# Performance work log

Measured on AMD Instinct MI355X. Metric: run time of the kernel, lower is better.

The kernel has to match this reference:

```python
import jax, jax.numpy as jnp
import numpy as np

B, S, MV = 32, 64, 30
V, E, H, L = 20000, 256, 512, 128
PAD_IDX = 0
THETA = 0.5


def setup_inputs() -> dict:
    key = jax.random.key(0)
    ks = jax.random.split(key, 12)
    sc = 0.02
    return {
        "z": jax.random.normal(ks[0], (B, L), jnp.float32),
        "input_sequence": jax.random.randint(ks[1], (B, S, MV), 0, V),
        "length": jax.random.randint(ks[2], (B,), 1, S + 1),
        "embedding_weight": jax.random.normal(ks[3], (V, E), jnp.float32) * sc,
        "W_l2h": jax.random.normal(ks[4], (H, L), jnp.float32) * sc,
        "b_l2h": jax.random.normal(ks[5], (H,), jnp.float32) * sc,
        "W_ih": jax.random.normal(ks[6], (3 * H, E), jnp.float32) * sc,
        "W_hh": jax.random.normal(ks[7], (3 * H, H), jnp.float32) * sc,
        "b_ih": jax.random.normal(ks[8], (3 * H,), jnp.float32) * sc,
        "b_hh": jax.random.normal(ks[9], (3 * H,), jnp.float32) * sc,
        "W_out": jax.random.normal(ks[10], (V, H), jnp.float32) * sc,
        "b_out": jax.random.normal(ks[11], (V,), jnp.float32) * sc,
    }


def _gru(emb, h0, W_ih, W_hh, b_ih, b_hh):
    # emb: (B,S,E); PyTorch GRU cell, single layer.
    def step(h, x_t):
        gi = x_t @ W_ih.T + b_ih          # (B,3H)
        gh = h @ W_hh.T + b_hh            # (B,3H)
        i_r, i_z, i_n = jnp.split(gi, 3, axis=-1)
        h_r, h_z, h_n = jnp.split(gh, 3, axis=-1)
        r = jax.nn.sigmoid(i_r + h_r)
        zt = jax.nn.sigmoid(i_z + h_z)
        n = jnp.tanh(i_n + r * h_n)
        h_new = (1.0 - zt) * n + zt * h
        return h_new, h_new
    _, outs = jax.lax.scan(step, h0, jnp.swapaxes(emb, 0, 1))  # (S,B,H)
    return jnp.swapaxes(outs, 0, 1)  # (B,S,H)


def reference(z, input_sequence, length, embedding_weight, W_l2h, b_l2h,
              W_ih, W_hh, b_ih, b_hh, W_out, b_out):
    # Multi-hot scatter: zeros.scatter_(2, idx, 1)
    mh = jnp.zeros((B, S, V), jnp.float32).at[
        jnp.arange(B)[:, None, None], jnp.arange(S)[None, :, None], input_sequence
    ].set(1.0)
    mh = mh.at[:, :, PAD_IDX].set(0.0)
    # Dense one-hot matmul embedding-sum (faithful to torch.mm on (B*S,V))
    emb = jnp.tanh(jnp.einsum('bsv,ve->bse', mh, embedding_weight))
    h0 = z @ W_l2h.T + b_l2h                      # (B,H)
    outputs = _gru(emb, h0, W_ih, W_hh, b_ih, b_hh)  # (B,S,H)
    # pack/pad semantics: outputs beyond each length are zero
    valid = jnp.arange(S)[None, :] < length[:, None]
    outputs = outputs * valid[..., None]
    m_output = jnp.sum(jnp.abs(outputs), axis=2) > 0  # (B,S) bool
    logits = jnp.einsum('bsh,vh->bsv', outputs, W_out) + b_out  # (B,S,V)
    p_output = jax.nn.sigmoid(logits)
    # _sample: top-k over logits[..., 3:], shift by 3, threshold via sigmoid
    top_p, top_i = jax.lax.top_k(logits[..., 3:], MV)
    top_i = top_i + 3
    s_output = jnp.where(jax.nn.sigmoid(top_p) <= THETA, PAD_IDX, top_i)  # (B,S,MV)
    return (p_output, s_output, m_output)
```

## Files before the change

### kernel.cpp

```cpp
#include <hip/hip_runtime.h>
#include <hip/hip_bf16.h>
#include <math.h>

#define B_ 32
#define S_ 64
#define MV_ 30
#define V_ 20000
#define E_ 256
#define H_ 512
#define L_ 128
#define H3_ 1536
#define BS_ 2048
#define NB4 256
#define NEG7 -3.0e38f
#define SENT 0xFFF8000000000000ULL

typedef __attribute__((ext_vector_type(8))) short short8v;
typedef __attribute__((ext_vector_type(4))) float f32x4;
typedef unsigned long long ull_;

__global__ __launch_bounds__(256) void k12(const int* __restrict__ seq,
                                           const float* __restrict__ Ew,
                                           const float* __restrict__ z,
                                           const float* __restrict__ Wl,
                                           const float* __restrict__ bl,
                                           double* __restrict__ emb,
                                           double* __restrict__ hstep) {
    __shared__ int sidx[MV_];
    int bid = blockIdx.x;
    int t = threadIdx.x;
    if (bid < BS_) {
        int row = bid;
        if (t < MV_) sidx[t] = seq[row * MV_ + t];
        __syncthreads();
        double acc = 0.0;
        for (int i = 0; i < MV_; ++i) {
            int id = sidx[i];
            if (id == 0) continue;
            bool dup = false;
            for (int q = 0; q < i; ++q) dup = dup || (sidx[q] == id);
            if (!dup) acc += (double)Ew[(size_t)id * E_ + t];
        }
        emb[(size_t)row * E_ + t] = tanh(acc);
    } else if (bid < BS_ + 64) {
        int o = (bid - BS_) * 256 + t;
        int b = o >> 9;
        int j = o & 511;
        const float4* zr = (const float4*)(z + (size_t)b * L_);
        const float4* wr = (const float4*)(Wl + (size_t)j * L_);
        double acc = (double)bl[j];
#pragma unroll
        for (int k = 0; k < L_ / 4; ++k) {
            float4 a = zr[k];
            float4 w = wr[k];
            acc += (double)a.x * (double)w.x + (double)a.y * (double)w.y
                 + (double)a.z * (double)w.z + (double)a.w * (double)w.w;
        }
        hstep[(size_t)(b >> 2) * 2048 + j * 4 + (b & 3)] = acc;
    } else {
        ull_* hs = (ull_*)hstep;
        size_t i = (size_t)(bid - (BS_ + 64)) * 1024 + (size_t)t * 4;
        hs[16384 + i + 0] = SENT;
        hs[16384 + i + 1] = SENT;
        hs[16384 + i + 2] = SENT;
        hs[16384 + i + 3] = SENT;
    }
}

__global__ __launch_bounds__(256) void k3_gi(const double* __restrict__ A,
                                             const float* __restrict__ Bm,
                                             const float* __restrict__ bih,
                                             double* __restrict__ gi) {
    __shared__ double As[16][66];
    __shared__ double Bs[16][66];
    int t = threadIdx.x;
    int n0 = blockIdx.x * 64;
    int m0 = blockIdx.y * 64;
    int tx = t & 15, ty = t >> 4;
    int ml = t >> 2;
    int kl = (t & 3) * 4;
    double acc[4][4];
#pragma unroll
    for (int i = 0; i < 4; ++i)
#pragma unroll
        for (int j = 0; j < 4; ++j) acc[i][j] = 0.0;

    for (int kt = 0; kt < 256; kt += 16) {
        double4 av = *(const double4*)(A + (size_t)(m0 + ml) * 256 + kt + kl);
        float4 bv = *(const float4*)(Bm + (size_t)(n0 + ml) * 256 + kt + kl);
        As[kl + 0][ml] = av.x; As[kl + 1][ml] = av.y; As[kl + 2][ml] = av.z; As[kl + 3][ml] = av.w;
        Bs[kl + 0][ml] = (double)bv.x; Bs[kl + 1][ml] = (double)bv.y;
        Bs[kl + 2][ml] = (double)bv.z; Bs[kl + 3][ml] = (double)bv.w;
        __syncthreads();
#pragma unroll
        for (int kk = 0; kk < 16; ++kk) {
            double2 a01 = *(const double2*)&As[kk][ty * 4];
            double2 a23 = *(const double2*)&As[kk][ty * 4 + 2];
            double2 b01 = *(const double2*)&Bs[kk][tx * 4];
            double2 b23 = *(const double2*)&Bs[kk][tx * 4 + 2];
            double am[4] = {a01.x, a01.y, a23.x, a23.y};
            double bn[4] = {b01.x, b01.y, b23.x, b23.y};
#pragma unroll
            for (int i = 0; i < 4; ++i)
#pragma unroll
                for (int j = 0; j < 4; ++j) acc[i][j] += am[i] * bn[j];
        }
        __syncthreads();
    }
#pragma unroll
    for (int i = 0; i < 4; ++i) {
        int m = m0 + ty * 4 + i;
        int bb = m >> 6, ss = m & 63;
#pragma unroll
        for (int j = 0; j < 4; ++j) {
            int n = n0 + tx * 4 + j;
            int g = n >> 9, u = n & 511;
            gi[(((size_t)(ss * 512 + u)) * 3 + g) * 32 + bb] = acc[i][j] + (double)bih[n];
        }
    }
}

__global__ __launch_bounds__(256, 1) void k4_gru(const double* __restrict__ gi,
                                                 const float* __restrict__ whh,
                                                 const float* __restrict__ bhh,
                                                 const int* __restrict__ length,
                                                 double* __restrict__ hstep,
                                                 float* __restrict__ outs,
                                                 short* __restrict__ A16) {
    __shared__ double hl[2112];
    __shared__ double part[2][4][16][13];

    int t = threadIdx.x;
    int wv = t >> 6;
    int lane = t & 63;
    int bid = blockIdx.x;
    int g = bid & 7;
    int beta = bid >> 3;

    int ul = lane >> 2, ks = lane & 3;

    const float* wbase = whh + ((size_t)(beta * 16 + ul)) * 512 + wv * 128 + ks * 32;
    float4 w0r[8], w1r[8], w2r[8];
#pragma unroll
    for (int c = 0; c < 8; ++c) {
        w0r[c] = *(const float4*)(wbase + c * 4);
        w1r[c] = *(const float4*)(wbase + 512 * 512 + c * 4);
        w2r[c] = *(const float4*)(wbase + 1024 * 512 + c * 4);
    }

    const double* hg0 = hstep + (size_t)g * 2048;
    {
#pragma unroll
        for (int j = 0; j < 8; ++j) {
            int e = t + j * 256;
            hl[e + ((e >> 7) << 2)] = hg0[e];
        }
    }
    __syncthreads();

    int u2 = lane >> 2, b2 = lane & 3;
    int u_g = beta * 16 + u2;
    int b_g = g * 4 + b2;
    double gr = 0.0, gz = 0.0, gn = 0.0, bhr_ = 0.0, bhz_ = 0.0, bhn_ = 0.0;
    double hv = 0.0;
    int len = 0;
    if (wv == 0) {
        bhr_ = (double)bhh[u_g];
        bhz_ = (double)bhh[u_g + 512];
        bhn_ = (double)bhh[u_g + 1024];
        len = length[b_g];
        hv = hg0[u_g * 4 + b2];
        size_t gb = ((size_t)u_g * 3) * 32 + b_g;
        gr = gi[gb]; gz = gi[gb + 32]; gn = gi[gb + 64];
    }

    const double* hr = &hl[(wv * 128 + ks * 32) * 4 + ((wv * 4 + ks) << 2)];

    for (int s = 0; s < S_; ++s) {
        int par = s & 1;
        ull_ ta[4], tb[4];
        const ull_* src = (const ull_*)(hstep + (size_t)s * 16384 + (size_t)g * 2048)
                          + wv * 512;
        if (s > 0) {
            while (true) {
                bool ok = true;
#pragma unroll
                for (int j = 0; j < 4; ++j) {
                    ta[j] = __hip_atomic_load(&src[(2 * j) * 64 + lane],
                                              __ATOMIC_RELAXED, __HIP_MEMORY_SCOPE_AGENT);
                    ok = ok && (ta[j] != SENT);
                }
                if (__all(ok)) break;
                __builtin_amdgcn_s_sleep(1);
            }
#pragma unroll
            for (int j = 0; j < 4; ++j)
                tb[j] = __hip_atomic_load(&src[(2 * j + 1) * 64 + lane],
                                          __ATOMIC_RELAXED, __HIP_MEMORY_SCOPE_AGENT);
            asm volatile("" ::: "memory");
            {
                ull_* hlu = (ull_*)hl;
#pragma unroll
                for (int j = 0; j < 4; ++j) {
                    int e = wv * 512 + (2 * j) * 64 + lane;
                    hlu[e + ((e >> 7) << 2)] = ta[j];
                }
            }
        }

        double a0[4] = {0, 0, 0, 0}, a1[4] = {0, 0, 0, 0}, a2[4] = {0, 0, 0, 0};
#pragma unroll
        for (int c = 0; c < 4; ++c) {
            const double* hp = hr + c * 16;
            double2 hA0 = *(const double2*)(hp + 0),  hB0 = *(const double2*)(hp + 2);
            double2 hA1 = *(const double2*)(hp + 4),  hB1 = *(const double2*)(hp + 6);
            double2 hA2 = *(const double2*)(hp + 8),  hB2 = *(const double2*)(hp + 10);
            double2 hA3 = *(const double2*)(hp + 12), hB3 = *(const double2*)(hp + 14);
            float4 w0 = w0r[c], w1 = w1r[c], w2 = w2r[c];
            { double d0 = (double)w0.x, d1 = (double)w1.x, d2 = (double)w2.x;
              a0[0] += hA0.x * d0; a0[1] += hA0.y * d0; a0[2] += hB0.x * d0; a0[3] += hB0.y * d0;
              a1[0] += hA0.x * d1; a1[1] += hA0.y * d1; a1[2] += hB0.x * d1; a1[3] += hB0.y * d1;
              a2[0] += hA0.x * d2; a2[1] += hA0.y * d2; a2[2] += hB0.x * d2; a2[3] += hB0.y * d2; }
            { double d0 = (double)w0.y, d1 = (double)w1.y, d2 = (double)w2.y;
              a0[0] += hA1.x * d0; a0[1] += hA1.y * d0; a0[2] += hB1.x * d0; a0[3] += hB1.y * d0;
              a1[0] += hA1.x * d1; a1[1] += hA1.y * d1; a1[2] += hB1.x * d1; a1[3] += hB1.y * d1;
              a2[0] += hA1.x * d2; a2[1] += hA1.y * d2; a2[2] += hB1.x * d2; a2[3] += hB1.y * d2; }
            { double d0 = (double)w0.z, d1 = (double)w1.z, d2 = (double)w2.z;
              a0[0] += hA2.x * d0; a0[1] += hA2.y * d0; a0[2] += hB2.x * d0; a0[3] += hB2.y * d0;
              a1[0] += hA2.x * d1; a1[1] += hA2.y * d1; a1[2] += hB2.x * d1; a1[3] += hB2.y * d1;
              a2[0] += hA2.x * d2; a2[1] += hA2.y * d2; a2[2] += hB2.x * d2; a2[3] += hB2.y * d2; }
            { double d0 = (double)w0.w, d1 = (double)w1.w, d2 = (double)w2.w;
              a0[0] += hA3.x * d0; a0[1] += hA3.y * d0; a0[2] += hB3.x * d0; a0[3] += hB3.y * d0;
              a1[0] += hA3.x * d1; a1[1] += hA3.y * d1; a1[2] += hB3.x * d1; a1[3] += hB3.y * d1;
              a2[0] += hA3.x * d2; a2[1] += hA3.y * d2; a2[2] += hB3.x * d2; a2[3] += hB3.y * d2; }
        }

        if (s > 0) {
            while (true) {
                bool ok = true;
#pragma unroll
                for (int j = 0; j < 4; ++j) ok = ok && (tb[j] != SENT);
                if (__all(ok)) break;
                __builtin_amdgcn_s_sleep(1);
#pragma unroll
                for (int j = 0; j < 4; ++j)
                    tb[j] = __hip_atomic_load(&src[(2 * j + 1) * 64 + lane],
                                              __ATOMIC_RELAXED, __HIP_MEMORY_SCOPE_AGENT);
            }
            asm volatile("" ::: "memory");
            {
                ull_* hlu = (ull_*)hl;
#pragma unroll
                for (int j = 0; j < 4; ++j) {
                    int e = wv * 512 + (2 * j + 1) * 64 + lane;
                    hlu[e + ((e >> 7) << 2)] = tb[j];
                }
            }
        }

#pragma unroll
        for (int c = 4; c < 8; ++c) {
            const double* hp = hr + c * 16;
            double2 hA0 = *(const double2*)(hp + 0),  hB0 = *(const double2*)(hp + 2);
            double2 hA1 = *(const double2*)(hp + 4),  hB1 = *(const double2*)(hp + 6);
            double2 hA2 = *(const double2*)(hp + 8),  hB2 = *(const double2*)(hp + 10);
            double2 hA3 = *(const double2*)(hp + 12), hB3 = *(const double2*)(hp + 14);
            float4 w0 = w0r[c], w1 = w1r[c], w2 = w2r[c];
            { double d0 = (double)w0.x, d1 = (double)w1.x, d2 = (double)w2.x;
              a0[0] += hA0.x * d0; a0[1] += hA0.y * d0; a0[2] += hB0.x * d0; a0[3] += hB0.y * d0;
              a1[0] += hA0.x * d1; a1[1] += hA0.y * d1; a1[2] += hB0.x * d1; a1[3] += hB0.y * d1;
              a2[0] += hA0.x * d2; a2[1] += hA0.y * d2; a2[2] += hB0.x * d2; a2[3] += hB0.y * d2; }
            { double d0 = (double)w0.y, d1 = (double)w1.y, d2 = (double)w2.y;
              a0[0] += hA1.x * d0; a0[1] += hA1.y * d0; a0[2] += hB1.x * d0; a0[3] += hB1.y * d0;
              a1[0] += hA1.x * d1; a1[1] += hA1.y * d1; a1[2] += hB1.x * d1; a1[3] += hB1.y * d1;
              a2[0] += hA1.x * d2; a2[1] += hA1.y * d2; a2[2] += hB1.x * d2; a2[3] += hB1.y * d2; }
            { double d0 = (double)w0.z, d1 = (double)w1.z, d2 = (double)w2.z;
              a0[0] += hA2.x * d0; a0[1] += hA2.y * d0; a0[2] += hB2.x * d0; a0[3] += hB2.y * d0;
              a1[0] += hA2.x * d1; a1[1] += hA2.y * d1; a1[2] += hB2.x * d1; a1[3] += hB2.y * d1;
              a2[0] += hA2.x * d2; a2[1] += hA2.y * d2; a2[2] += hB2.x * d2; a2[3] += hB2.y * d2; }
            { double d0 = (double)w0.w, d1 = (double)w1.w, d2 = (double)w2.w;
              a0[0] += hA3.x * d0; a0[1] += hA3.y * d0; a0[2] += hB3.x * d0; a0[3] += hB3.y * d0;
              a1[0] += hA3.x * d1; a1[1] += hA3.y * d1; a1[2] += hB3.x * d1; a1[3] += hB3.y * d1;
              a2[0] += hA3.x * d2; a2[1] += hA3.y * d2; a2[2] += hB3.x * d2; a2[3] += hB3.y * d2; }
        }

#pragma unroll
        for (int b = 0; b < 4; ++b) {
            a0[b] += __shfl_xor(a0[b], 1); a0[b] += __shfl_xor(a0[b], 2);
            a1[b] += __shfl_xor(a1[b], 1); a1[b] += __shfl_xor(a1[b], 2);
            a2[b] += __shfl_xor(a2[b], 1); a2[b] += __shfl_xor(a2[b], 2);
        }
        if (ks == 0) {
#pragma unroll
            for (int b = 0; b < 4; ++b) {
                part[par][wv][ul][0 * 4 + b] = a0[b];
                part[par][wv][ul][1 * 4 + b] = a1[b];
                part[par][wv][ul][2 * 4 + b] = a2[b];
            }
        }
        __syncthreads();

        if (wv == 0) {
            double s0 = part[par][0][u2][0 * 4 + b2] + part[par][1][u2][0 * 4 + b2]
                      + part[par][2][u2][0 * 4 + b2] + part[par][3][u2][0 * 4 + b2];
            double s1 = part[par][0][u2][1 * 4 + b2] + part[par][1][u2][1 * 4 + b2]
                      + part[par][2][u2][1 * 4 + b2] + part[par][3][u2][1 * 4 + b2];
            double s2 = part[par][0][u2][2 * 4 + b2] + part[par][1][u2][2 * 4 + b2]
                      + part[par][2][u2][2 * 4 + b2] + part[par][3][u2][2 * 4 + b2];
            double r  = 1.0 / (1.0 + exp(-(gr + s0 + bhr_)));
            double zt = 1.0 / (1.0 + exp(-(gz + s1 + bhz_)));
            double n  = tanh(gn + r * (s2 + bhn_));
            double hn_ = (1.0 - zt) * n + zt * hv;
            hv = hn_;
            if (s < S_ - 1) {
                ull_* hdst = (ull_*)(hstep + (size_t)(s + 1) * 16384 + (size_t)g * 2048);
                __hip_atomic_store(&hdst[beta * 64 + lane],
                                   __builtin_bit_cast(ull_, hn_),
                                   __ATOMIC_RELAXED, __HIP_MEMORY_SCOPE_AGENT);
                size_t gb = ((size_t)((s + 1) * 512 + u_g) * 3) * 32 + b_g;
                gr = gi[gb]; gz = gi[gb + 32]; gn = gi[gb + 64];
            }
            float ov = (s < len) ? (float)hn_ : 0.0f;
            size_t oidx = (size_t)(b_g * 64 + s) * H_ + u_g;
            outs[oidx] = ov;
            {
                unsigned u = __builtin_bit_cast(unsigned, ov);
                A16[oidx] = (short)((u + 0x7FFFu + ((u >> 16) & 1u)) >> 16);
            }
        }
    }
}

__device__ __forceinline__ unsigned short f2b_(float x) {
    unsigned u = __builtin_bit_cast(unsigned, x);
    return (unsigned short)((u + 0x7FFFu + ((u >> 16) & 1u)) >> 16);
}
__device__ __forceinline__ short8v pack8_(float4 a, float4 b) {
    short8v r;
    r[0] = (short)f2b_(a.x); r[1] = (short)f2b_(a.y);
    r[2] = (short)f2b_(a.z); r[3] = (short)f2b_(a.w);
    r[4] = (short)f2b_(b.x); r[5] = (short)f2b_(b.y);
    r[6] = (short)f2b_(b.z); r[7] = (short)f2b_(b.w);
    return r;
}
__global__ __launch_bounds__(256) void k_prep2(const float* __restrict__ Wsrc,
                                               short* __restrict__ W16) {
    int i = blockIdx.x * 256 + threadIdx.x;
    float4 a = *(const float4*)&Wsrc[(size_t)i * 8];
    float4 b = *(const float4*)&Wsrc[(size_t)i * 8 + 4];
    *(short8v*)&W16[(size_t)i * 8] = pack8_(a, b);
}

#define LDK5 72
__global__ __launch_bounds__(256, 2) void k5_mfma(const short* __restrict__ A16,
                                                  const short* __restrict__ W16,
                                                  const float* __restrict__ bo,
                                                  float* __restrict__ pOut) {
    __shared__ short As[128 * LDK5];
    __shared__ short Bs[128 * LDK5];
    int t = threadIdx.x;
    int bid = blockIdx.x;
    int swz = (bid & 7) * 314 + (bid >> 3);
    int m0 = (swz & 15) * 128;
    int n0 = (swz >> 4) * 128;
    int lane = t & 63, wv = t >> 6;
    int wr = wv >> 1, wc = wv & 1;
    int ml = t >> 1;
    int kl = (t & 1) * 32;

    const short* Arow = A16 + (size_t)(m0 + ml) * H_ + kl;
    int vrow = n0 + ml;
    bool vok = vrow < V_;
    const short* Wrow = W16 + (size_t)(vok ? vrow : 0) * H_ + kl;
    short8v zz = (short8v){0, 0, 0, 0, 0, 0, 0, 0};

    f32x4 acc[4][4];
#pragma unroll
    for (int i = 0; i < 4; ++i)
#pragma unroll
        for (int j = 0; j < 4; ++j) acc[i][j] = (f32x4){0.f, 0.f, 0.f, 0.f};

    int ko = lane >> 4;
    int rr = lane & 15;

    for (int kt = 0; kt < H_; kt += 64) {
        short8v a0 = *(const short8v*)(Arow + kt);
        short8v a1 = *(const short8v*)(Arow + kt + 8);
        short8v a2 = *(const short8v*)(Arow + kt + 16);
        short8v a3 = *(const short8v*)(Arow + kt + 24);
        short8v b0 = vok ? *(const short8v*)(Wrow + kt) : zz;
        short8v b1 = vok ? *(const short8v*)(Wrow + kt + 8) : zz;
        short8v b2 = vok ? *(const short8v*)(Wrow + kt + 16) : zz;
        short8v b3 = vok ? *(const short8v*)(Wrow + kt + 24) : zz;
        *(short8v*)&As[ml * LDK5 + kl]      = a0;
        *(short8v*)&As[ml * LDK5 + kl + 8]  = a1;
        *(short8v*)&As[ml * LDK5 + kl + 16] = a2;
        *(short8v*)&As[ml * LDK5 + kl + 24] = a3;
        *(short8v*)&Bs[ml * LDK5 + kl]      = b0;
        *(short8v*)&Bs[ml * LDK5 + kl + 8]  = b1;
        *(short8v*)&Bs[ml * LDK5 + kl + 16] = b2;
        *(short8v*)&Bs[ml * LDK5 + kl + 24] = b3;
        __syncthreads();

#pragma unroll
        for (int kh = 0; kh < 2; ++kh) {
            short8v af[4], bf[4];
#pragma unroll
            for (int i = 0; i < 4; ++i)
                af[i] = *(const short8v*)&As[(wr * 64 + i * 16 + rr) * LDK5 + kh * 32 + ko * 8];
#pragma unroll
            for (int j = 0; j < 4; ++j)
                bf[j] = *(const short8v*)&Bs[(wc * 64 + j * 16 + rr) * LDK5 + kh * 32 + ko * 8];
#pragma unroll
            for (int i = 0; i < 4; ++i)
#pragma unroll
                for (int j = 0; j < 4; ++j)
                    acc[i][j] = __builtin_amdgcn_mfma_f32_16x16x32_bf16(af[i], bf[j], acc[i][j], 0, 0, 0);
        }
        __syncthreads();
    }

    int cr4 = (lane >> 4) * 4;
    float bov[4];
#pragma unroll
    for (int j = 0; j < 4; ++j) {
        int v = n0 + wc * 64 + j * 16 + rr;
        bov[j] = (v < V_) ? bo[v] : 0.f;
    }
#pragma unroll
    for (int i = 0; i < 4; ++i) {
#pragma unroll
        for (int j = 0; j < 4; ++j) {
            int v = n0 + wc * 64 + j * 16 + rr;
            if (v < V_) {
#pragma unroll
                for (int r = 0; r < 4; ++r) {
                    int m = m0 + wr * 64 + i * 16 + cr4 + r;
                    float x = acc[i][j][r] + bov[j];
                    pOut[(size_t)m * V_ + v] = 1.0f / (1.0f + expf(-x));
                }
            }
        }
    }
}

__global__ __launch_bounds__(512) void k7a_cand(const float* __restrict__ pOut,
                                                float* __restrict__ candV,
                                                int* __restrict__ candI) {
    int row = blockIdx.x;
    int t = threadIdx.x;
    int wv = t >> 6;
    int lane = t & 63;
    const float* rowp = pOut + (size_t)row * V_ + wv * 2500;

    float rv[40];
#pragma unroll
    for (int q4 = 0; q4 < 10; ++q4) {
        int base = q4 * 256 + lane * 4;
        float4 v4 = *(const float4*)(rowp + base);
        float vv[4] = {v4.x, v4.y, v4.z, v4.w};
#pragma unroll
        for (int c = 0; c < 4; ++c) {
            int li = base + c;
            int col = wv * 2500 + li;
            bool ok = (li < 2500) && (col >= 3);
            rv[q4 * 4 + c] = ok ? vv[c] : NEG7;
        }
    }
    float m1 = rv[0]; int s1 = 0;
#pragma unroll
    for (int q = 1; q < 40; ++q)
        if (rv[q] > m1) { m1 = rv[q]; s1 = q; }
    float m2 = NEG7; int s2 = 0;
#pragma unroll
    for (int q = 0; q < 40; ++q)
        if (q != s1 && rv[q] > m2) { m2 = rv[q]; s2 = q; }
    bool dirty = false;
    ull_ used = 0;
    int myidx = wv * 2500 + (s1 >> 2) * 256 + lane * 4 + (s1 & 3);

    float keepv = NEG7; int keepi = 0;
#pragma unroll 1
    for (int r = 0; r < 32; ++r) {
        float bv = m1; int bi = myidx;
#pragma unroll
        for (int m = 1; m < 64; m <<= 1) {
            float ov = __shfl_xor(bv, m);
            int   oi = __shfl_xor(bi, m);
            if (ov > bv || (ov == bv && oi < bi)) { bv = ov; bi = oi; }
        }
        if (lane == r) { keepv = bv; keepi = bi; }
        if (myidx == bi) {
            used |= (1ull << s1);
            if (!dirty) {
                m1 = m2; s1 = s2; dirty = true;
            } else {
                m1 = NEG7; s1 = 0;
#pragma unroll
                for (int q = 0; q < 40; ++q) {
                    float v = ((used >> q) & 1ull) ? NEG7 : rv[q];
                    if (v > m1) { m1 = v; s1 = q; }
                }
                m2 = NEG7; s2 = 0;
#pragma unroll
                for (int q = 0; q < 40; ++q) {
                    float v = (((used >> q) & 1ull) || q == s1) ? NEG7 : rv[q];
                    if (v > m2) { m2 = v; s2 = q; }
                }
                dirty = false;
            }
            myidx = wv * 2500 + (s1 >> 2) * 256 + lane * 4 + (s1 & 3);
        }
    }
    if (lane < 32) {
        size_t o = ((size_t)row * 8 + wv) * 32 + lane;
        candV[o] = keepv;
        candI[o] = keepi;
    }
}

__global__ __launch_bounds__(256) void k7b_final(const float* __restrict__ candV,
                                                 const int* __restrict__ candI,
                                                 const float* __restrict__ outs,
                                                 const float* __restrict__ W,
                                                 const float* __restrict__ bo,
                                                 float* __restrict__ mOut,
                                                 float* __restrict__ sOut) {
    __shared__ float selv[64];
    __shared__ int   seli[64];
    __shared__ float resv[64];
    __shared__ float redm[4];
    __shared__ __align__(16) float orow[H_];

    int row = blockIdx.x;
    int t = threadIdx.x;
    int lane = t & 63, wid = t >> 6;

    if (wid != 0) {
        for (int i = t - 64; i < H_; i += 192)
            orow[i] = outs[(size_t)row * H_ + i];
    } else {
        float cv[4]; int ci[4];
#pragma unroll
        for (int q = 0; q < 4; ++q) {
            size_t o = (size_t)row * 256 + q * 64 + lane;
            cv[q] = candV[o];
            ci[q] = candI[o];
        }
        float lv = cv[0]; int lix = ci[0]; int ls = 0;
#pragma unroll
        for (int q = 1; q < 4; ++q)
            if (cv[q] > lv || (cv[q] == lv && ci[q] < lix)) { lv = cv[q]; lix = ci[q]; ls = q; }

#pragma unroll 1
        for (int r = 0; r < 64; ++r) {
            float bv = lv; int bi = lix;
#pragma unroll
            for (int m = 1; m < 64; m <<= 1) {
                float ov = __shfl_xor(bv, m);
                int   oi = __shfl_xor(bi, m);
                if (ov > bv || (ov == bv && oi < bi)) { bv = ov; bi = oi; }
            }
            if (lane == r) { selv[r] = bv; seli[r] = bi; }
            if (lix == bi) {
#pragma unroll
                for (int q = 0; q < 4; ++q) cv[q] = (ls == q) ? NEG7 : cv[q];
                lv = cv[0]; lix = ci[0]; ls = 0;
#pragma unroll
                for (int q = 1; q < 4; ++q)
                    if (cv[q] > lv || (cv[q] == lv && ci[q] < lix)) { lv = cv[q]; lix = ci[q]; ls = q; }
            }
        }
    }
    __syncthreads();

    {
        float ms = fabsf(orow[t]) + fabsf(orow[t + 256]);
#pragma unroll
        for (int m = 1; m < 64; m <<= 1) ms += __shfl_xor(ms, m);
        if (lane == 0) redm[wid] = ms;
    }

    {
        int c = t >> 2, q = t & 3;
        int gidx = seli[c];
        const float4* w4 = (const float4*)(W + (size_t)gidx * H_);
        const float4* o4 = (const float4*)orow;
        double acc = 0.0;
#pragma unroll 8
        for (int i2 = 0; i2 < 32; ++i2) {
            float4 wv4 = w4[i2 * 4 + q];
            float4 ov4 = o4[i2 * 4 + q];
            acc += (double)wv4.x * (double)ov4.x + (double)wv4.y * (double)ov4.y
                 + (double)wv4.z * (double)ov4.z + (double)wv4.w * (double)ov4.w;
        }
        acc += __shfl_xor(acc, 1);
        acc += __shfl_xor(acc, 2);
        if (q == 0) resv[c] = (float)(acc + (double)bo[gidx]);
    }
    __syncthreads();

    if (t == 0)
        mOut[row] = (redm[0] + redm[1] + redm[2] + redm[3] > 0.f) ? 1.f : 0.f;

    if (t < 64) {
        float v = resv[t];
        int idx = seli[t];
#pragma unroll 1
        for (int r = 0; r < MV_; ++r) {
            float bv = v; int bi = idx;
#pragma unroll
            for (int m = 1; m < 64; m <<= 1) {
                float ov = __shfl_xor(bv, m);
                int   oi = __shfl_xor(bi, m);
                if (ov > bv || (ov == bv && oi < bi)) { bv = ov; bi = oi; }
            }
            if (t == 0)
                sOut[(size_t)row * MV_ + r] = (bv <= 0.0f) ? 0.0f : (float)bi;
            if (idx == bi) v = NEG7;
        }
    }
}

extern "C" void kernel_launch(void* const* d_in, const int* in_sizes, int n_in,
                              void* d_out, int out_size, void* d_ws, size_t ws_size,
                              hipStream_t stream) {
    const float* z      = (const float*)d_in[0];
    const int*   seq    = (const int*)d_in[1];
    const int*   length = (const int*)d_in[2];
    const float* Ew     = (const float*)d_in[3];
    const float* W_l2h  = (const float*)d_in[4];
    const float* b_l2h  = (const float*)d_in[5];
    const float* W_ih   = (const float*)d_in[6];
    const float* W_hh   = (const float*)d_in[7];
    const float* b_ih   = (const float*)d_in[8];
    const float* b_hh   = (const float*)d_in[9];
    const float* W_out  = (const float*)d_in[10];
    const float* b_out  = (const float*)d_in[11];

    float* out = (float*)d_out;

    double* emb_d = (double*)d_ws;
    double* gi_d  = emb_d + 524288;
    double* hstep = gi_d + 3145728;
    float*  outs  = (float*)(hstep + 1048576);
    float*  candV = outs + 1048576;
    int*    candI = (int*)(candV + (size_t)BS_ * 256);
    short*  A16   = (short*)emb_d;
    short*  W16   = (short*)gi_d;

    float* pOut = out;
    float* sOut = out + (size_t)BS_ * V_;
    float* mOut = sOut + (size_t)BS_ * MV_;

    k12<<<BS_ + 64 + 1008, 256, 0, stream>>>(seq, Ew, z, W_l2h, b_l2h, emb_d, hstep);
    k3_gi<<<dim3(24, 32), 256, 0, stream>>>(emb_d, W_ih, b_ih, gi_d);
    k4_gru<<<NB4, 256, 0, stream>>>(gi_d, W_hh, b_hh, length, hstep, outs, A16);
    k_prep2<<<5000, 256, 0, stream>>>(W_out, W16);
    k5_mfma<<<2512, 256, 0, stream>>>(A16, W16, b_out, pOut);
    k7a_cand<<<BS_, 512, 0, stream>>>(pOut, candV, candI);
    k7b_final<<<BS_, 256, 0, stream>>>(candV, candI, outs, W_out, b_out, mOut, sOut);
}
```

Baseline: 659.7 us.

## Widen output GEMM tile to 128x256 and fuse top-k candidate and final kernels

The logits GEMM now computes 128x256 tiles per block, so each wave holds 4x8 MFMA accumulators and each thread stages a full 64-wide K slice of one W row. This halves the block count and increases reuse of the A tile. The two-stage top-k is merged into one 512-thread kernel that keeps the per-wave candidates in shared memory instead of a global buffer, removing a launch and a global round-trip. The larger accumulator set raises register pressure, which may lower occupancy.

```diff
diff --git a/kernel.cpp b/kernel.cpp
--- a/kernel.cpp
+++ b/kernel.cpp
@@ -357,28 +357,28 @@
                                                   const float* __restrict__ bo,
                                                   float* __restrict__ pOut) {
     __shared__ short As[128 * LDK5];
-    __shared__ short Bs[128 * LDK5];
+    __shared__ short Bs[256 * LDK5];
     int t = threadIdx.x;
     int bid = blockIdx.x;
-    int swz = (bid & 7) * 314 + (bid >> 3);
+    int swz = (bid & 7) * 158 + (bid >> 3);
     int m0 = (swz & 15) * 128;
-    int n0 = (swz >> 4) * 128;
+    int n0 = (swz >> 4) * 256;
     int lane = t & 63, wv = t >> 6;
     int wr = wv >> 1, wc = wv & 1;
     int ml = t >> 1;
     int kl = (t & 1) * 32;
 
     const short* Arow = A16 + (size_t)(m0 + ml) * H_ + kl;
-    int vrow = n0 + ml;
+    int vrow = n0 + t;
     bool vok = vrow < V_;
-    const short* Wrow = W16 + (size_t)(vok ? vrow : 0) * H_ + kl;
+    const short* Wrow = W16 + (size_t)(vok ? vrow : 0) * H_;
     short8v zz = (short8v){0, 0, 0, 0, 0, 0, 0, 0};
 
-    f32x4 acc[4][4];
+    f32x4 acc[4][8];
 #pragma unroll
     for (int i = 0; i < 4; ++i)
 #pragma unroll
-        for (int j = 0; j < 4; ++j) acc[i][j] = (f32x4){0.f, 0.f, 0.f, 0.f};
+        for (int j = 0; j < 8; ++j) acc[i][j] = (f32x4){0.f, 0.f, 0.f, 0.f};
 
     int ko = lane >> 4;
     int rr = lane & 15;
@@ -388,50 +388,49 @@
         short8v a1 = *(const short8v*)(Arow + kt + 8);
         short8v a2 = *(const short8v*)(Arow + kt + 16);
         short8v a3 = *(const short8v*)(Arow + kt + 24);
-        short8v b0 = vok ? *(const short8v*)(Wrow + kt) : zz;
-        short8v b1 = vok ? *(const short8v*)(Wrow + kt + 8) : zz;
-        short8v b2 = vok ? *(const short8v*)(Wrow + kt + 16) : zz;
-        short8v b3 = vok ? *(const short8v*)(Wrow + kt + 24) : zz;
+        short8v bb[8];
+#pragma unroll
+        for (int jj = 0; jj < 8; ++jj)
+            bb[jj] = vok ? *(const short8v*)(Wrow + kt + jj * 8) : zz;
         *(short8v*)&As[ml * LDK5 + kl]      = a0;
         *(short8v*)&As[ml * LDK5 + kl + 8]  = a1;
         *(short8v*)&As[ml * LDK5 + kl + 16] = a2;
         *(short8v*)&As[ml * LDK5 + kl + 24] = a3;
-        *(short8v*)&Bs[ml * LDK5 + kl]      = b0;
-        *(short8v*)&Bs[ml * LDK5 + kl + 8]  = b1;
-        *(short8v*)&Bs[ml * LDK5 + kl + 16] = b2;
-        *(short8v*)&Bs[ml * LDK5 + kl + 24] = b3;
+#pragma unroll
+        for (int jj = 0; jj < 8; ++jj)
+            *(short8v*)&Bs[t * LDK5 + jj * 8] = bb[jj];
         __syncthreads();
 
 #pragma unroll
         for (int kh = 0; kh < 2; ++kh) {
-            short8v af[4], bf[4];
+            short8v af[4], bf[8];
 #pragma unroll
             for (int i = 0; i < 4; ++i)
                 af[i] = *(const short8v*)&As[(wr * 64 + i * 16 + rr) * LDK5 + kh * 32 + ko * 8];
 #pragma unroll
-            for (int j = 0; j < 4; ++j)
-                bf[j] = *(const short8v*)&Bs[(wc * 64 + j * 16 + rr) * LDK5 + kh * 32 + ko * 8];
+            for (int j = 0; j < 8; ++j)
+                bf[j] = *(const short8v*)&Bs[(wc * 128 + j * 16 + rr) * LDK5 + kh * 32 + ko * 8];
 #pragma unroll
             for (int i = 0; i < 4; ++i)
 #pragma unroll
-                for (int j = 0; j < 4; ++j)
+                for (int j = 0; j < 8; ++j)
                     acc[i][j] = __builtin_amdgcn_mfma_f32_16x16x32_bf16(af[i], bf[j], acc[i][j], 0, 0, 0);
         }
         __syncthreads();
     }
 
     int cr4 = (lane >> 4) * 4;
-    float bov[4];
-#pragma unroll
-    for (int j = 0; j < 4; ++j) {
-        int v = n0 + wc * 64 + j * 16 + rr;
+    float bov[8];
+#pragma unroll
+    for (int j = 0; j < 8; ++j) {
+        int v = n0 + wc * 128 + j * 16 + rr;
         bov[j] = (v < V_) ? bo[v] : 0.f;
     }
 #pragma unroll
     for (int i = 0; i < 4; ++i) {
 #pragma unroll
-        for (int j = 0; j < 4; ++j) {
-            int v = n0 + wc * 64 + j * 16 + rr;
+        for (int j = 0; j < 8; ++j) {
+            int v = n0 + wc * 128 + j * 16 + rr;
             if (v < V_) {
 #pragma unroll
                 for (int r = 0; r < 4; ++r) {
@@ -444,88 +443,14 @@
     }
 }
 
-__global__ __launch_bounds__(512) void k7a_cand(const float* __restrict__ pOut,
-                                                float* __restrict__ candV,
-                                                int* __restrict__ candI) {
-    int row = blockIdx.x;
-    int t = threadIdx.x;
-    int wv = t >> 6;
-    int lane = t & 63;
-    const float* rowp = pOut + (size_t)row * V_ + wv * 2500;
-
-    float rv[40];
-#pragma unroll
-    for (int q4 = 0; q4 < 10; ++q4) {
-        int base = q4 * 256 + lane * 4;
-        float4 v4 = *(const float4*)(rowp + base);
-        float vv[4] = {v4.x, v4.y, v4.z, v4.w};
-#pragma unroll
-        for (int c = 0; c < 4; ++c) {
-            int li = base + c;
-            int col = wv * 2500 + li;
-            bool ok = (li < 2500) && (col >= 3);
-            rv[q4 * 4 + c] = ok ? vv[c] : NEG7;
-        }
-    }
-    float m1 = rv[0]; int s1 = 0;
-#pragma unroll
-    for (int q = 1; q < 40; ++q)
-        if (rv[q] > m1) { m1 = rv[q]; s1 = q; }
-    float m2 = NEG7; int s2 = 0;
-#pragma unroll
-    for (int q = 0; q < 40; ++q)
-        if (q != s1 && rv[q] > m2) { m2 = rv[q]; s2 = q; }
-    bool dirty = false;
-    ull_ used = 0;
-    int myidx = wv * 2500 + (s1 >> 2) * 256 + lane * 4 + (s1 & 3);
-
-    float keepv = NEG7; int keepi = 0;
-#pragma unroll 1
-    for (int r = 0; r < 32; ++r) {
-        float bv = m1; int bi = myidx;
-#pragma unroll
-        for (int m = 1; m < 64; m <<= 1) {
-            float ov = __shfl_xor(bv, m);
-            int   oi = __shfl_xor(bi, m);
-            if (ov > bv || (ov == bv && oi < bi)) { bv = ov; bi = oi; }
-        }
-        if (lane == r) { keepv = bv; keepi = bi; }
-        if (myidx == bi) {
-            used |= (1ull << s1);
-            if (!dirty) {
-                m1 = m2; s1 = s2; dirty = true;
-            } else {
-                m1 = NEG7; s1 = 0;
-#pragma unroll
-                for (int q = 0; q < 40; ++q) {
-                    float v = ((used >> q) & 1ull) ? NEG7 : rv[q];
-                    if (v > m1) { m1 = v; s1 = q; }
-                }
-                m2 = NEG7; s2 = 0;
-#pragma unroll
-                for (int q = 0; q < 40; ++q) {
-                    float v = (((used >> q) & 1ull) || q == s1) ? NEG7 : rv[q];
-                    if (v > m2) { m2 = v; s2 = q; }
-                }
-                dirty = false;
-            }
-            myidx = wv * 2500 + (s1 >> 2) * 256 + lane * 4 + (s1 & 3);
-        }
-    }
-    if (lane < 32) {
-        size_t o = ((size_t)row * 8 + wv) * 32 + lane;
-        candV[o] = keepv;
-        candI[o] = keepi;
-    }
-}
-
-__global__ __launch_bounds__(256) void k7b_final(const float* __restrict__ candV,
-                                                 const int* __restrict__ candI,
-                                                 const float* __restrict__ outs,
-                                                 const float* __restrict__ W,
-                                                 const float* __restrict__ bo,
-                                                 float* __restrict__ mOut,
-                                                 float* __restrict__ sOut) {
+__global__ __launch_bounds__(512) void k7_top(const float* __restrict__ pOut,
+                                              const float* __restrict__ outs,
+                                              const float* __restrict__ W,
+                                              const float* __restrict__ bo,
+                                              float* __restrict__ mOut,
+                                              float* __restrict__ sOut) {
+    __shared__ float candVl[256];
+    __shared__ int   candIl[256];
     __shared__ float selv[64];
     __shared__ int   seli[64];
     __shared__ float resv[64];
@@ -534,33 +459,102 @@
 
     int row = blockIdx.x;
     int t = threadIdx.x;
-    int lane = t & 63, wid = t >> 6;
-
-    if (wid != 0) {
-        for (int i = t - 64; i < H_; i += 192)
-            orow[i] = outs[(size_t)row * H_ + i];
-    } else {
-        float cv[4]; int ci[4];
-#pragma unroll
-        for (int q = 0; q < 4; ++q) {
-            size_t o = (size_t)row * 256 + q * 64 + lane;
-            cv[q] = candV[o];
-            ci[q] = candI[o];
-        }
-        float lv = cv[0]; int lix = ci[0]; int ls = 0;
-#pragma unroll
-        for (int q = 1; q < 4; ++q)
-            if (cv[q] > lv || (cv[q] == lv && ci[q] < lix)) { lv = cv[q]; lix = ci[q]; ls = q; }
-
+    int wv = t >> 6;
+    int lane = t & 63;
+    int wid = wv;
+
+    {
+        const float* rowp = pOut + (size_t)row * V_ + wv * 2500;
+        float rv[40];
+#pragma unroll
+        for (int q4 = 0; q4 < 10; ++q4) {
+            int base = q4 * 256 + lane * 4;
+            float4 v4 = *(const float4*)(rowp + base);
+            float vv[4] = {v4.x, v4.y, v4.z, v4.w};
+#pragma unroll
+            for (int c = 0; c < 4; ++c) {
+                int li = base + c;
+                int col = wv * 2500 + li;
+                bool ok = (li < 2500) && (col >= 3);
+                rv[q4 * 4 + c] = ok ? vv[c] : NEG7;
+            }
+        }
+        float m1 = rv[0]; int s1 = 0;
+#pragma unroll
+        for (int q = 1; q < 40; ++q)
+            if (rv[q] > m1) { m1 = rv[q]; s1 = q; }
+        float m2 = NEG7; int s2 = 0;
+#pragma unroll
+        for (int q = 0; q < 40; ++q)
+            if (q != s1 && rv[q] > m2) { m2 = rv[q]; s2 = q; }
+        bool dirty = false;
+        ull_ used = 0;
+        int myidx = wv * 2500 + (s1 >> 2) * 256 + lane * 4 + (s1 & 3);
+
+        float keepv = NEG7; int keepi = 0;
 #pragma unroll 1
-        for (int r = 0; r < 64; ++r) {
-            float bv = lv; int bi = lix;
+        for (int r = 0; r < 32; ++r) {
+            float bv = m1; int bi = myidx;
 #pragma unroll
             for (int m = 1; m < 64; m <<= 1) {
                 float ov = __shfl_xor(bv, m);
                 int   oi = __shfl_xor(bi, m);
                 if (ov > bv || (ov == bv && oi < bi)) { bv = ov; bi = oi; }
             }
+            if (lane == r) { keepv = bv; keepi = bi; }
+            if (myidx == bi) {
+                used |= (1ull << s1);
+                if (!dirty) {
+                    m1 = m2; s1 = s2; dirty = true;
+                } else {
+                    m1 = NEG7; s1 = 0;
+#pragma unroll
+                    for (int q = 0; q < 40; ++q) {
+                        float v = ((used >> q) & 1ull) ? NEG7 : rv[q];
+                        if (v > m1) { m1 = v; s1 = q; }
+                    }
+                    m2 = NEG7; s2 = 0;
+#pragma unroll
+                    for (int q = 0; q < 40; ++q) {
+                        float v = (((used >> q) & 1ull) || q == s1) ? NEG7 : rv[q];
+                        if (v > m2) { m2 = v; s2 = q; }
+                    }
+                    dirty = false;
+                }
+                myidx = wv * 2500 + (s1 >> 2) * 256 + lane * 4 + (s1 & 3);
+            }
+        }
+        if (lane < 32) {
+            candVl[wv * 32 + lane] = keepv;
+            candIl[wv * 32 + lane] = keepi;
+        }
+    }
+    __syncthreads();
+
+    if (t >= 64 && t < 256) {
+        for (int i = t - 64; i < H_; i += 192)
+            orow[i] = outs[(size_t)row * H_ + i];
+    } else if (t < 64) {
+        float cv[4]; int ci[4];
+#pragma unroll
+        for (int q = 0; q < 4; ++q) {
+            cv[q] = candVl[q * 64 + lane];
+            ci[q] = candIl[q * 64 + lane];
+        }
+        float lv = cv[0]; int lix = ci[0]; int ls = 0;
+#pragma unroll
+        for (int q = 1; q < 4; ++q)
+            if (cv[q] > lv || (cv[q] == lv && ci[q] < lix)) { lv = cv[q]; lix = ci[q]; ls = q; }
+
+#pragma unroll 1
+        for (int r = 0; r < 64; ++r) {
+            float bv = lv; int bi = lix;
+#pragma unroll
+            for (int m = 1; m < 64; m <<= 1) {
+                float ov = __shfl_xor(bv, m);
+                int   oi = __shfl_xor(bi, m);
+                if (ov > bv || (ov == bv && oi < bi)) { bv = ov; bi = oi; }
+            }
             if (lane == r) { selv[r] = bv; seli[r] = bi; }
             if (lix == bi) {
 #pragma unroll
@@ -574,14 +568,14 @@
     }
     __syncthreads();
 
-    {
+    if (t < 256) {
         float ms = fabsf(orow[t]) + fabsf(orow[t + 256]);
 #pragma unroll
         for (int m = 1; m < 64; m <<= 1) ms += __shfl_xor(ms, m);
         if (lane == 0) redm[wid] = ms;
     }
 
-    {
+    if (t < 256) {
         int c = t >> 2, q = t & 3;
         int gidx = seli[c];
         const float4* w4 = (const float4*)(W + (size_t)gidx * H_);
@@ -644,8 +638,6 @@
     double* gi_d  = emb_d + 524288;
     double* hstep = gi_d + 3145728;
     float*  outs  = (float*)(hstep + 1048576);
-    float*  candV = outs + 1048576;
-    int*    candI = (int*)(candV + (size_t)BS_ * 256);
     short*  A16   = (short*)emb_d;
     short*  W16   = (short*)gi_d;
 
@@ -657,7 +649,6 @@
     k3_gi<<<dim3(24, 32), 256, 0, stream>>>(emb_d, W_ih, b_ih, gi_d);
     k4_gru<<<NB4, 256, 0, stream>>>(gi_d, W_hh, b_hh, length, hstep, outs, A16);
     k_prep2<<<5000, 256, 0, stream>>>(W_out, W16);
-    k5_mfma<<<2512, 256, 0, stream>>>(A16, W16, b_out, pOut);
-    k7a_cand<<<BS_, 512, 0, stream>>>(pOut, candV, candI);
-    k7b_final<<<BS_, 256, 0, stream>>>(candV, candI, outs, W_out, b_out, mOut, sOut);
-}
+    k5_mfma<<<1264, 256, 0, stream>>>(A16, W16, b_out, pOut);
+    k7_top<<<BS_, 512, 0, stream>>>(pOut, outs, W_out, b_out, mOut, sOut);
+}
```

New measurement: 884.3 us. 34.1% more time.
